# Kernel tuning notes

Hardware: AMD Instinct MI355X
Metric: run time of the kernel (lower is better)

Reference implementation:

```python
import jax, jax.numpy as jnp
import numpy as np

B, T, D = 32, 1024, 1024
H = D // 2  # hidden per direction


def setup_inputs() -> dict:
    key = jax.random.key(0)
    ks = jax.random.split(key, 8)
    s_in = 1.0 / np.sqrt(D).astype(np.float32)
    s_h = 1.0 / np.sqrt(H).astype(np.float32)
    return {
        "x": jax.random.normal(ks[0], (B, T, D), jnp.float32),
        "Wx_f": jax.random.normal(ks[1], (D, 4 * H), jnp.float32) * s_in,
        "Wh_f": jax.random.normal(ks[2], (H, 4 * H), jnp.float32) * s_h,
        "b_f": jnp.zeros((4 * H,), jnp.float32),
        "Wx_b": jax.random.normal(ks[3], (D, 4 * H), jnp.float32) * s_in,
        "Wh_b": jax.random.normal(ks[4], (H, 4 * H), jnp.float32) * s_h,
        "b_b": jnp.zeros((4 * H,), jnp.float32),
        "W_fc": jax.random.normal(ks[5], (2 * H, 1), jnp.float32) * (1.0 / np.sqrt(2 * H).astype(np.float32)),
        "b_fc": jnp.zeros((1,), jnp.float32),
    }


def _lstm_dir(x_tm, Wx, Wh, b):
    # x_tm: [T, B, D] time-major. Standard LSTM, gate order (i, f, g, o).
    Bn = x_tm.shape[1]
    Hh = Wh.shape[0]
    # Precompute input projections for all timesteps in one big GEMM.
    xg = jnp.einsum('tbd,dg->tbg', x_tm, Wx) + b  # [T, B, 4H]

    def step(carry, xg_t):
        h, c = carry
        g = xg_t + h @ Wh  # [B, 4H]
        i, f, gg, o = jnp.split(g, 4, axis=-1)
        i = jax.nn.sigmoid(i)
        f = jax.nn.sigmoid(f)
        gg = jnp.tanh(gg)
        o = jax.nn.sigmoid(o)
        c = f * c + i * gg
        h = o * jnp.tanh(c)
        return (h, c), h

    init = (jnp.zeros((Bn, Hh), x_tm.dtype), jnp.zeros((Bn, Hh), x_tm.dtype))
    _, hs = jax.lax.scan(step, init, xg)
    return hs  # [T, B, H]


def reference(x, Wx_f, Wh_f, b_f, Wx_b, Wh_b, b_b, W_fc, b_fc):
    xt = jnp.transpose(x, (1, 0, 2))  # [T, B, D]
    h_fwd = _lstm_dir(xt, Wx_f, Wh_f, b_f)              # [T, B, H]
    h_bwd = _lstm_dir(xt[::-1], Wx_b, Wh_b, b_b)[::-1]  # [T, B, H]
    h = jnp.concatenate([h_fwd, h_bwd], axis=-1)        # [T, B, 2H]
    logits = jnp.einsum('tbh,h->tb', h, W_fc[:, 0]) + b_fc[0]
    out = jax.nn.sigmoid(logits)                        # [T, B]
    return jnp.transpose(out)                           # [B, T]
```

## Files before the change

kernel.cpp:

```cpp
#include <hip/hip_runtime.h>
#include <hip/hip_bf16.h>
#include <cstdint>
#include <cstddef>

#define TT 1024
#define BB 32
#define DD 1024
#define HH 512
#define GG 2048

#define POISON_U64 0xFC00FC00FC00FC00ull

typedef _Float16 f16x8 __attribute__((ext_vector_type(8)));
typedef _Float16 f16x4 __attribute__((ext_vector_type(4)));
typedef float    f32x4 __attribute__((ext_vector_type(4)));

__device__ __forceinline__ float sigm(float x) { return 1.0f / (1.0f + __expf(-x)); }
__device__ __forceinline__ float tanh_fast(float x) { return 2.0f / (1.0f + __expf(-2.0f * x)) - 1.0f; }

__global__ __launch_bounds__(256) void init_kernel(unsigned long long* __restrict__ hr) {
    const int i = blockIdx.x * 256 + threadIdx.x;
    const int slot = (i >> 11) & 3;
    hr[i] = (slot == 0) ? 0ull : POISON_U64;
}

__global__ __launch_bounds__(256) void transpose_f16(const float* __restrict__ in,
                                                     _Float16* __restrict__ out,
                                                     int K, int N) {
    __shared__ float tile[32][33];
    const int tx = threadIdx.x & 31, ty = threadIdx.x >> 5;
    const int n0 = blockIdx.x * 32, k0 = blockIdx.y * 32;
#pragma unroll
    for (int j = 0; j < 4; j++)
        tile[ty + 8 * j][tx] = in[(size_t)(k0 + ty + 8 * j) * N + n0 + tx];
    __syncthreads();
#pragma unroll
    for (int j = 0; j < 4; j++)
        out[(size_t)(n0 + ty + 8 * j) * K + k0 + tx] = (_Float16)tile[tx][ty + 8 * j];
}

__global__ __launch_bounds__(256) void gemm_xg(const float* __restrict__ x,
                                               const _Float16* __restrict__ WxT_f,
                                               const float* __restrict__ b_f,
                                               const _Float16* __restrict__ WxT_b,
                                               const float* __restrict__ b_b,
                                               _Float16* __restrict__ xg_f,
                                               _Float16* __restrict__ xg_b) {
    const int dir = blockIdx.z;
    const _Float16* __restrict__ WxT = dir ? WxT_b : WxT_f;
    const float* __restrict__ bias = dir ? b_b : b_f;
    _Float16* __restrict__ out = dir ? xg_b : xg_f;

    const int n0 = blockIdx.x * 128;
    const int m0 = blockIdx.y * 128;

    __shared__ _Float16 A_lds[128 * 72];
    __shared__ _Float16 B_lds[128 * 72];

    const int tid = threadIdx.x;
    const int wave = tid >> 6;
    const int lane = tid & 63;
    const int jn = lane & 15;
    const int quad = lane >> 4;

    f32x4 acc[2][8] = {};

    for (int k0 = 0; k0 < DD; k0 += 64) {
        {
            const int kq = tid & 15;
            const int mq = tid >> 4;
#pragma unroll
            for (int i = 0; i < 8; i++) {
                const int m = mq + 16 * i;
                const int gm = m0 + m;
                const int t = gm >> 5;
                const int b = gm & 31;
                const float4 v = *(const float4*)(x + ((size_t)b * TT + t) * DD + k0 + kq * 4);
                f16x4 f;
                f.x = (_Float16)v.x; f.y = (_Float16)v.y;
                f.z = (_Float16)v.z; f.w = (_Float16)v.w;
                *(f16x4*)(A_lds + m * 72 + kq * 4) = f;
            }
        }
        {
            const int kq = tid & 7;
            const int nq = tid >> 3;
#pragma unroll
            for (int i = 0; i < 4; i++) {
                const int n = nq + 32 * i;
                f16x8 w = *(const f16x8*)(WxT + (size_t)(n0 + n) * DD + k0 + kq * 8);
                *(f16x8*)(B_lds + n * 72 + kq * 8) = w;
            }
        }
        __syncthreads();
#pragma unroll
        for (int kc = 0; kc < 64; kc += 32) {
            const f16x8 a0 = *(const f16x8*)(A_lds + (wave * 32 + jn) * 72 + kc + quad * 8);
            const f16x8 a1 = *(const f16x8*)(A_lds + (wave * 32 + 16 + jn) * 72 + kc + quad * 8);
#pragma unroll
            for (int nt = 0; nt < 8; nt++) {
                const f16x8 bb = *(const f16x8*)(B_lds + (nt * 16 + jn) * 72 + kc + quad * 8);
                acc[0][nt] = __builtin_amdgcn_mfma_f32_16x16x32_f16(a0, bb, acc[0][nt], 0, 0, 0);
                acc[1][nt] = __builtin_amdgcn_mfma_f32_16x16x32_f16(a1, bb, acc[1][nt], 0, 0, 0);
            }
        }
        __syncthreads();
    }

    const int g = n0 >> 9;
    const int blkbase = (n0 & 511) >> 4;
    float bv[8];
#pragma unroll
    for (int nt = 0; nt < 8; nt++) bv[nt] = bias[n0 + nt * 16 + jn];
#pragma unroll
    for (int mt = 0; mt < 2; mt++) {
#pragma unroll
        for (int r = 0; r < 4; r++) {
            const int m = m0 + wave * 32 + mt * 16 + quad * 4 + r;
            const int t = m >> 5;
            const int b = m & 31;
            const int sidx = dir ? (1023 - t) : t;
            const int sc = sidx >> 3, si = sidx & 7;
#pragma unroll
            for (int nt = 0; nt < 8; nt++) {
                const int blk = blkbase + nt;
                const float val = acc[mt][nt][r] + bv[nt];
                const size_t idx =
                    ((((size_t)(blk * 32 + b) * 16 + jn) * 128 + sc) * 8 + si) * 4 + g;
                out[idx] = (_Float16)val;
            }
        }
    }
}

__global__ __launch_bounds__(512) void lstm_persist(
    const _Float16* __restrict__ xg_f,
    const _Float16* __restrict__ xg_b,
    const _Float16* __restrict__ WhT_f,
    const _Float16* __restrict__ WhT_b,
    const float* __restrict__ wfc,
    unsigned long long* __restrict__ hring,
    _Float16* __restrict__ part) {

    __shared__ __align__(16) _Float16 h_lds[16 * 520];
    __shared__ float red[4 * 16 * 33];

    const int tid = threadIdx.x;
    const int bid = blockIdx.x;
    const int dir = bid >> 5;
    const int grp = (bid >> 4) & 1;
    const int blk = bid & 15;

    const _Float16* __restrict__ xg = dir ? xg_b : xg_f;
    const _Float16* __restrict__ WhT = dir ? WhT_b : WhT_f;
    unsigned long long* hp = hring + ((size_t)(dir * 2 + grp)) * 8192;

    const int lane = tid & 63;
    const int wave = tid >> 6;
    const int g = wave >> 1;
    const int half = wave & 1;
    const int jl16 = lane & 15;
    const int quad = lane >> 4;

    f16x8 bfrag[16];
    {
        const _Float16* wcol = WhT + (size_t)(g * 512 + blk * 32 + half * 16 + jl16) * HH;
#pragma unroll
        for (int i = 0; i < 16; i++)
            bfrag[i] = *(const f16x8*)(wcol + i * 32 + quad * 8);
    }

    const int gb = tid >> 5;
    const int gc = tid & 31;
    float c_reg = 0.0f;
    const float wfc_reg = wfc[dir * 512 + blk * 32 + gc];

    unsigned long long* hl64 = (unsigned long long*)h_lds;
    const int blk32 = blk * 2 + (gc >> 4);
    const int b_glob = grp * 16 + gb;
    const _Float16* xbase =
        xg + (((size_t)(blk32 * 32 + b_glob) * 16 + (gc & 15)) * 128) * 32;

    const int prod_idx = gb * 128 + blk * 8 + (gc >> 2);
    const bool is_prod = ((gc & 3) == 0);

    f16x8 xcur[4];
    {
        const f16x8* src0 = (const f16x8*)(xbase);
#pragma unroll
        for (int q = 0; q < 4; q++) xcur[q] = src0[q];
    }

    for (int sc = 0; sc < 128; sc++) {
        f16x8 xnxt[4];
        if (sc < 127) {
            const f16x8* srcn = (const f16x8*)(xbase + (sc + 1) * 32);
#pragma unroll
            for (int q = 0; q < 4; q++) xnxt[q] = srcn[q];
        }

#pragma unroll
        for (int si = 0; si < 8; si++) {
            const int s = sc * 8 + si;
            const int t = dir ? (1023 - s) : s;

            if (s >= 2 && is_prod)
                __hip_atomic_store(hp + (size_t)((s - 2) & 3) * 2048 + prod_idx,
                                   POISON_U64, __ATOMIC_RELAXED,
                                   __HIP_MEMORY_SCOPE_AGENT);

            {
                const unsigned long long* __restrict__ src =
                    hp + (size_t)(s & 3) * 2048;
                unsigned int pend = 0xFu;
                int guard = 0;
                do {
                    unsigned long long v[4];
#pragma unroll
                    for (int q = 0; q < 4; q++)
                        if (pend & (1u << q))
                            v[q] = __hip_atomic_load(src + q * 512 + tid,
                                                     __ATOMIC_RELAXED,
                                                     __HIP_MEMORY_SCOPE_AGENT);
                    unsigned int got = 0;
#pragma unroll
                    for (int q = 0; q < 4; q++) {
                        if ((pend & (1u << q)) &&
                            ((unsigned int)v[q] & 0xFFFFu) != 0xFC00u) {
                            const int idx = q * 512 + tid;
                            hl64[(idx >> 7) * 130 + (idx & 127)] = v[q];
                            got |= (1u << q);
                        }
                    }
                    pend &= ~got;
                    if (pend) {
                        if (got == 0) __builtin_amdgcn_s_sleep(1);
                        if (++guard > (1 << 18)) break;
                    }
                } while (pend);
            }
            __syncthreads();

            {
                f32x4 a0 = {0.f, 0.f, 0.f, 0.f};
                f32x4 a1 = {0.f, 0.f, 0.f, 0.f};
                f32x4 a2 = {0.f, 0.f, 0.f, 0.f};
                f32x4 a3 = {0.f, 0.f, 0.f, 0.f};
                const _Float16* hrow = h_lds + jl16 * 520 + quad * 8;
#pragma unroll
                for (int i = 0; i < 4; i++) {
                    const f16x8 h0 = *(const f16x8*)(hrow + 32 * i);
                    const f16x8 h1 = *(const f16x8*)(hrow + 32 * (i + 4));
                    const f16x8 h2 = *(const f16x8*)(hrow + 32 * (i + 8));
                    const f16x8 h3 = *(const f16x8*)(hrow + 32 * (i + 12));
                    a0 = __builtin_amdgcn_mfma_f32_16x16x32_f16(h0, bfrag[i],      a0, 0, 0, 0);
                    a1 = __builtin_amdgcn_mfma_f32_16x16x32_f16(h1, bfrag[i + 4],  a1, 0, 0, 0);
                    a2 = __builtin_amdgcn_mfma_f32_16x16x32_f16(h2, bfrag[i + 8],  a2, 0, 0, 0);
                    a3 = __builtin_amdgcn_mfma_f32_16x16x32_f16(h3, bfrag[i + 12], a3, 0, 0, 0);
                }
                const f32x4 acc = (a0 + a1) + (a2 + a3);
#pragma unroll
                for (int r = 0; r < 4; r++)
                    red[(g * 16 + quad * 4 + r) * 33 + half * 16 + jl16] = acc[r];
            }
            __syncthreads();

            {
                const float p0 = red[(0 * 16 + gb) * 33 + gc] + (float)xcur[si >> 1][(si & 1) * 4 + 0];
                const float p1 = red[(1 * 16 + gb) * 33 + gc] + (float)xcur[si >> 1][(si & 1) * 4 + 1];
                const float p2 = red[(2 * 16 + gb) * 33 + gc] + (float)xcur[si >> 1][(si & 1) * 4 + 2];
                const float p3 = red[(3 * 16 + gb) * 33 + gc] + (float)xcur[si >> 1][(si & 1) * 4 + 3];

                const float gi = sigm(p0);
                const float gf = sigm(p1);
                const float gc_ = tanh_fast(p2);
                const float go = sigm(p3);
                c_reg = gf * c_reg + gi * gc_;
                const float hval = go * tanh_fast(c_reg);

                const float hnb = __shfl_xor(hval, 1);
                union { struct { _Float16 lo, hi; } h; unsigned int u; } cvt;
                cvt.h.lo = (_Float16)hval;
                cvt.h.hi = (_Float16)hnb;
                const unsigned int pair2 = __shfl_xor(cvt.u, 2);
                if (is_prod) {
                    const unsigned long long pv =
                        ((unsigned long long)pair2 << 32) | (unsigned long long)cvt.u;
                    __hip_atomic_store(hp + (size_t)((s + 1) & 3) * 2048 + prod_idx, pv,
                                       __ATOMIC_RELAXED, __HIP_MEMORY_SCOPE_AGENT);
                }
                float contrib = hval * wfc_reg;
                contrib += __shfl_xor(contrib, 1);
                contrib += __shfl_xor(contrib, 2);
                contrib += __shfl_xor(contrib, 4);
                contrib += __shfl_xor(contrib, 8);
                contrib += __shfl_xor(contrib, 16);
                if (gc == 0)
                    part[(size_t)(t * 32 + b_glob) * 32 + dir * 16 + blk] = (_Float16)contrib;
            }
        }

        if (sc < 127) {
#pragma unroll
            for (int q = 0; q < 4; q++) xcur[q] = xnxt[q];
        }
    }
}

__global__ __launch_bounds__(256) void fc_final(const _Float16* __restrict__ part,
                                                const float* __restrict__ b_fc,
                                                float* __restrict__ out) {
    const int i = blockIdx.x * 256 + threadIdx.x;
    const int b = i >> 10;
    const int t = i & 1023;
    const f16x8* p = (const f16x8*)(part + (size_t)(t * 32 + b) * 32);
    float acc = b_fc[0];
#pragma unroll
    for (int q = 0; q < 4; q++) {
        const f16x8 v = p[q];
#pragma unroll
        for (int e = 0; e < 8; e++) acc += (float)v[e];
    }
    out[i] = sigm(acc);
}

extern "C" void kernel_launch(void* const* d_in, const int* in_sizes, int n_in,
                              void* d_out, int out_size, void* d_ws, size_t ws_size,
                              hipStream_t stream) {
    const float* x    = (const float*)d_in[0];
    const float* Wx_f = (const float*)d_in[1];
    const float* Wh_f = (const float*)d_in[2];
    const float* b_f  = (const float*)d_in[3];
    const float* Wx_b = (const float*)d_in[4];
    const float* Wh_b = (const float*)d_in[5];
    const float* b_b  = (const float*)d_in[6];
    const float* W_fc = (const float*)d_in[7];
    const float* b_fc = (const float*)d_in[8];
    float* out = (float*)d_out;

    const size_t XG       = 134217728ULL;
    const size_t WXT_OFF  = 2 * XG;
    const size_t WHT_OFF  = WXT_OFF + 2 * 4194304ULL;
    const size_t need     = WHT_OFF + 2 * 2097152ULL;
    if (ws_size < need) return;

    uint8_t* ws = (uint8_t*)d_ws;
    _Float16* xg_f = (_Float16*)ws;
    _Float16* xg_b = (_Float16*)(ws + XG);
    _Float16* WxT_f = (_Float16*)(ws + WXT_OFF);
    _Float16* WxT_b = (_Float16*)(ws + WXT_OFF + 4194304ULL);
    _Float16* WhT_f = (_Float16*)(ws + WHT_OFF);
    _Float16* WhT_b = (_Float16*)(ws + WHT_OFF + 2097152ULL);
    _Float16* part  = (_Float16*)(ws + WXT_OFF);
    unsigned long long* hring =
        (unsigned long long*)(ws + WXT_OFF + 4194304ULL);

    transpose_f16<<<dim3(64, 32), 256, 0, stream>>>(Wx_f, WxT_f, 1024, 2048);
    transpose_f16<<<dim3(64, 32), 256, 0, stream>>>(Wx_b, WxT_b, 1024, 2048);
    transpose_f16<<<dim3(64, 16), 256, 0, stream>>>(Wh_f, WhT_f, 512, 2048);
    transpose_f16<<<dim3(64, 16), 256, 0, stream>>>(Wh_b, WhT_b, 512, 2048);

    gemm_xg<<<dim3(16, 256, 2), 256, 0, stream>>>(
        x, WxT_f, b_f, WxT_b, b_b, xg_f, xg_b);

    init_kernel<<<128, 256, 0, stream>>>(hring);

    lstm_persist<<<64, 512, 0, stream>>>(
        xg_f, xg_b, WhT_f, WhT_b, W_fc, hring, part);

    fc_final<<<(BB * TT) / 256, 256, 0, stream>>>(part, b_fc, out);
}
```

Baseline: 3.830 ms.

## Regroup xg GEMM columns across gates and stage output through LDS for vectorized stores

```diff
diff --git a/kernel.cpp b/kernel.cpp
--- a/kernel.cpp
+++ b/kernel.cpp
@@ -51,11 +51,13 @@
     const float* __restrict__ bias = dir ? b_b : b_f;
     _Float16* __restrict__ out = dir ? xg_b : xg_f;
 
-    const int n0 = blockIdx.x * 128;
+    const int c0 = blockIdx.x * 32;
     const int m0 = blockIdx.y * 128;
 
-    __shared__ _Float16 A_lds[128 * 72];
-    __shared__ _Float16 B_lds[128 * 72];
+    __shared__ __align__(16) unsigned char smem[40960];
+    _Float16* A_lds = (_Float16*)smem;
+    _Float16* B_lds = (_Float16*)(smem + 18432);
+    _Float16* stage = (_Float16*)smem;
 
     const int tid = threadIdx.x;
     const int wave = tid >> 6;
@@ -87,9 +89,11 @@
             const int nq = tid >> 3;
 #pragma unroll
             for (int i = 0; i < 4; i++) {
-                const int n = nq + 32 * i;
-                f16x8 w = *(const f16x8*)(WxT + (size_t)(n0 + n) * DD + k0 + kq * 8);
-                *(f16x8*)(B_lds + n * 72 + kq * 8) = w;
+                const int nl = nq + 32 * i;
+                const int g = nl >> 5;
+                const int c = nl & 31;
+                f16x8 w = *(const f16x8*)(WxT + (size_t)(g * 512 + c0 + c) * DD + k0 + kq * 8);
+                *(f16x8*)(B_lds + nl * 72 + kq * 8) = w;
             }
         }
         __syncthreads();
@@ -107,29 +111,43 @@
         __syncthreads();
     }
 
-    const int g = n0 >> 9;
-    const int blkbase = (n0 & 511) >> 4;
     float bv[8];
 #pragma unroll
-    for (int nt = 0; nt < 8; nt++) bv[nt] = bias[n0 + nt * 16 + jn];
+    for (int nt = 0; nt < 8; nt++)
+        bv[nt] = bias[(nt >> 1) * 512 + c0 + (nt & 1) * 16 + jn];
+
+    const int lsi = dir ? (3 - wave) : wave;
 #pragma unroll
     for (int mt = 0; mt < 2; mt++) {
 #pragma unroll
         for (int r = 0; r < 4; r++) {
-            const int m = m0 + wave * 32 + mt * 16 + quad * 4 + r;
-            const int t = m >> 5;
-            const int b = m & 31;
-            const int sidx = dir ? (1023 - t) : t;
-            const int sc = sidx >> 3, si = sidx & 7;
+            const int b = mt * 16 + quad * 4 + r;
 #pragma unroll
             for (int nt = 0; nt < 8; nt++) {
-                const int blk = blkbase + nt;
-                const float val = acc[mt][nt][r] + bv[nt];
-                const size_t idx =
-                    ((((size_t)(blk * 32 + b) * 16 + jn) * 128 + sc) * 8 + si) * 4 + g;
-                out[idx] = (_Float16)val;
-            }
-        }
+                const int c = (nt & 1) * 16 + jn;
+                stage[c * 520 + b * 16 + lsi * 4 + (nt >> 1)] =
+                    (_Float16)(acc[mt][nt][r] + bv[nt]);
+            }
+        }
+    }
+    __syncthreads();
+
+    const int sidx0 = dir ? (1020 - blockIdx.y * 4) : (blockIdx.y * 4);
+    const int sc = sidx0 >> 3;
+    const int si0 = sidx0 & 7;
+#pragma unroll
+    for (int it = 0; it < 4; it++) {
+        const int p = it * 256 + tid;
+        const int c = p & 31;
+        const int b = p >> 5;
+        const int cglob = c0 + c;
+        const int blk = cglob >> 4;
+        const int jl = cglob & 15;
+        const f16x8* srcp = (const f16x8*)(stage + c * 520 + b * 16);
+        const size_t obase =
+            ((((size_t)(blk * 32 + b) * 16 + jl) * 128 + sc) * 8 + si0) * 4;
+        *(f16x8*)(out + obase) = srcp[0];
+        *(f16x8*)(out + obase + 8) = srcp[1];
     }
 }
 
```

Result: faster. 3.372 ms (-12.0%).
